# Optimization experiments

Measured on AMD Instinct MI355X. Metric: run time of the kernel, lower is better.

## Reference

```python
import jax, jax.numpy as jnp
import numpy as np

LEAKY_SLOPE = 0.01

def bilinear_interpolate(grid, coords):
    # grid: [H, W, C]; coords: [N, 2] in [0,1] (x, y order as in torch code)
    H = grid.shape[0] - 1
    W = grid.shape[1] - 1
    fx = coords[:, 0] * W
    fy = coords[:, 1] * H
    x0 = fx.astype(jnp.int32)
    y0 = fy.astype(jnp.int32)
    xf = jnp.mod(fx, 1.0)
    yf = jnp.mod(fy, 1.0)
    x1 = jnp.minimum(x0 + 1, W)
    y1 = jnp.minimum(y0 + 1, H)
    tl = grid[y0, x0]  # [N, C]
    tr = grid[y0, x1]
    bl = grid[y1, x0]
    br = grid[y1, x1]
    xf = xf[:, None]
    yf = yf[:, None]
    top = (1.0 - xf) * tl + xf * tr
    bot = (1.0 - xf) * bl + xf * br
    return (1.0 - yf) * top + yf * bot


def setup_inputs() -> dict:
    key = jax.random.key(0)
    ks = jax.random.split(key, 10)
    N = 2097152
    pos = jax.random.uniform(ks[0], (N, 2), dtype=jnp.float32)
    dir = jax.random.uniform(ks[1], (N, 2), dtype=jnp.float32)
    pos_grid = jax.random.normal(ks[2], (256, 256, 3), dtype=jnp.float32) * 10.0
    dir_grid = jax.random.normal(ks[3], (256, 256, 3), dtype=jnp.float32) * 10.0
    # Linear layers: PyTorch default init U(-1/sqrt(fan_in), 1/sqrt(fan_in))
    def linear(kw, kb, fan_in, fan_out):
        bound = 1.0 / np.sqrt(fan_in)
        W = jax.random.uniform(kw, (fan_out, fan_in), minval=-bound, maxval=bound, dtype=jnp.float32)
        b = jax.random.uniform(kb, (fan_out,), minval=-bound, maxval=bound, dtype=jnp.float32)
        return W, b
    W1, b1 = linear(ks[4], ks[5], 6, 64)
    W2, b2 = linear(ks[6], ks[7], 64, 64)
    W3, b3 = linear(ks[8], ks[9], 64, 1)
    return {"pos": pos, "dir": dir, "pos_grid": pos_grid, "dir_grid": dir_grid,
            "W1": W1, "b1": b1, "W2": W2, "b2": b2, "W3": W3, "b3": b3}


def reference(pos, dir, pos_grid, dir_grid, W1, b1, W2, b2, W3, b3):
    pos_feat = jax.lax.stop_gradient(bilinear_interpolate(pos_grid, pos))  # .detach() in torch
    dir_feat = jax.lax.stop_gradient(bilinear_interpolate(dir_grid, dir))
    x = jnp.concatenate([pos_feat, dir_feat], axis=1)  # [N, 6]
    x = jax.nn.leaky_relu(x @ W1.T + b1, LEAKY_SLOPE)
    x = jax.nn.leaky_relu(x @ W2.T + b2, LEAKY_SLOPE)
    return jax.nn.sigmoid(x @ W3.T + b3)  # [N, 1]
```

## Files before the change

### kernel.cpp

```cpp
#include <hip/hip_runtime.h>
#include <hip/hip_bf16.h>
#include <math.h>


#define NTHREADS 256
#define NB 4

typedef __attribute__((ext_vector_type(4))) short s16x4;
typedef __attribute__((ext_vector_type(8))) short s16x8;
typedef __attribute__((ext_vector_type(8))) __bf16 bf16x8;
typedef __attribute__((ext_vector_type(4))) float f32x4;
typedef __attribute__((ext_vector_type(4))) int i32x4;
typedef __attribute__((ext_vector_type(2))) int i32x2;

static __device__ __forceinline__ short f2bf(float f) {
    return __builtin_bit_cast(short, __float2bfloat16(f));
}
static __device__ __forceinline__ int pk2(float lo, float hi) {
    unsigned short l = (unsigned short)f2bf(lo);
    unsigned short h = (unsigned short)f2bf(hi);
    return (int)(((unsigned int)h << 16) | (unsigned int)l);
}
static __device__ __forceinline__ int cvt_pk_bf16(float a, float b) {
    int r;
    asm("v_cvt_pk_bf16_f32 %0, %1, %2" : "=v"(r) : "v"(a), "v"(b));
    return r;
}
static __device__ __forceinline__ float bflo(int u) {
    return __builtin_bit_cast(float, u << 16);
}
static __device__ __forceinline__ float bfhi(int u) {
    return __builtin_bit_cast(float, (int)(u & 0xffff0000));
}
static __device__ __forceinline__ int opaq(int x) {
    asm volatile("" : "+v"(x));
    return x;
}

__global__ __launch_bounds__(256) void make_patches(
    const float* __restrict__ gP, const float* __restrict__ gD,
    int* __restrict__ outP, int* __restrict__ outD) {
    int gid = blockIdx.x * 256 + threadIdx.x;
    const float* g = (gid < 65536) ? gP : gD;
    int* po = (gid < 65536) ? outP : outD;
    int id = gid & 65535;
    int y0 = id >> 8, x0 = id & 255;
    int x1 = min(x0 + 1, 255), y1 = min(y0 + 1, 255);
    const float* tl = g + (y0 * 256 + x0) * 3;
    const float* tr = g + (y0 * 256 + x1) * 3;
    const float* bl = g + (y1 * 256 + x0) * 3;
    const float* br = g + (y1 * 256 + x1) * 3;
    i32x4 u0;
    i32x2 u1;
    u0[0] = pk2(tl[0], bl[0]);
    u0[1] = pk2(tl[1], bl[1]);
    u0[2] = pk2(tl[2], bl[2]);
    u0[3] = pk2(tr[0], br[0]);
    u1[0] = pk2(tr[1], br[1]);
    u1[1] = pk2(tr[2], br[2]);
    *(i32x4*)(po + id * 8) = u0;
    *(i32x2*)(po + id * 8 + 4) = u1;
}

static __device__ __forceinline__ void patch_issue(
    const int* __restrict__ tab, float px, float py, int* P, float& xf,
    float& yf) {
    float fx = px * 255.0f;
    float fy = py * 255.0f;
    int x0 = (int)fx;
    int y0 = (int)fy;
    xf = fx - floorf(fx);
    yf = fy - floorf(fy);
    int idx = (y0 << 8) | x0;
    i32x4 a = *(const i32x4*)(tab + idx * 8);
    i32x2 b = *(const i32x2*)(tab + idx * 8 + 4);
    P[0] = a[0]; P[1] = a[1]; P[2] = a[2];
    P[3] = a[3]; P[4] = b[0]; P[5] = b[1];
}

static __device__ __forceinline__ void patch_lerp(const int* P, float xf,
                                                  float yf, float* f) {
#pragma unroll
    for (int ch = 0; ch < 3; ++ch) {
        float tl = bflo(P[ch]), bl = bfhi(P[ch]);
        float tr = bflo(P[ch + 3]), br = bfhi(P[ch + 3]);
        float top = fmaf(xf, tr - tl, tl);
        float bot = fmaf(xf, br - bl, bl);
        f[ch] = fmaf(yf, bot - top, top);
    }
}

__global__ __launch_bounds__(NTHREADS, 4) void mlp_mfma_kernel(
    const float* __restrict__ pos, const float* __restrict__ dir,
    const int* __restrict__ patP, const int* __restrict__ patD,
    const float* __restrict__ W1, const float* __restrict__ b1,
    const float* __restrict__ W2, const float* __restrict__ b2,
    const float* __restrict__ W3, const float* __restrict__ b3,
    float* __restrict__ out) {
    __shared__ int lds_F[4 * 2 * 64 * 4];
    __shared__ __align__(16) float cw[128];

    const int tid = threadIdx.x;
    if (tid < 128) cw[tid] = (tid < 64) ? b2[tid] : W3[tid - 64];
    __syncthreads();

    const int w = tid >> 6;
    const int lane = tid & 63;
    const int c = lane & 15;
    const int q = lane >> 4;
    const int q4 = q * 4;

    int* FB = lds_F + w * (2 * 64 * 4);

    s16x4 A1f[4];
#pragma unroll
    for (int mt = 0; mt < 4; ++mt) {
        int f = mt * 16 + c;
        s16x4 t;
#pragma unroll
        for (int j = 0; j < 4; ++j) {
            int k = q4 + j;
            float v = 0.0f;
            if (k < 6) v = W1[f * 6 + k];
            else if (k == 6) v = b1[f];
            t[j] = f2bf(v);
        }
        A1f[mt] = t;
    }
    s16x8 A2f[2][4];
#pragma unroll
    for (int kt2 = 0; kt2 < 2; ++kt2)
#pragma unroll
        for (int mt = 0; mt < 4; ++mt) {
            int n2 = mt * 16 + c;
            s16x8 t;
#pragma unroll
            for (int j2 = 0; j2 < 8; ++j2) {
                int k = kt2 * 32 + ((j2 >> 2) * 16) + q4 + (j2 & 3);
                t[j2] = f2bf(W2[n2 * 64 + k]);
            }
            A2f[kt2][mt] = t;
        }
    const float b3s = b3[0];
    const int dbias = pk2(1.0f, 0.0f);
    const f32x4 zacc = {0.f, 0.f, 0.f, 0.f};

    const long wave_global = (long)blockIdx.x * 4 + w;
    const long base0 = wave_global * (64L * NB);
    const float2* pos2 = (const float2*)pos;
    const float2* dir2 = (const float2*)dir;

    float2 cp1, cd1;
    {
        float2 c0p = pos2[base0 + lane], c0d = dir2[base0 + lane];
        cp1 = pos2[base0 + 64 + lane];
        cd1 = dir2[base0 + 64 + lane];
        int P0_[12];
        float fr0[4];
        patch_issue(patP, c0p.x, c0p.y, P0_, fr0[0], fr0[1]);
        patch_issue(patD, c0d.x, c0d.y, P0_ + 6, fr0[2], fr0[3]);
        float feat[6];
        patch_lerp(P0_, fr0[0], fr0[1], feat);
        patch_lerp(P0_ + 6, fr0[2], fr0[3], feat + 3);
        i32x4 dv;
        dv[0] = cvt_pk_bf16(feat[0], feat[1]);
        dv[1] = cvt_pk_bf16(feat[2], feat[3]);
        dv[2] = cvt_pk_bf16(feat[4], feat[5]);
        dv[3] = dbias;
        *(i32x4*)(FB + lane * 4) = dv;
    }

#pragma unroll 1
    for (int ib = 0; ib < NB; ++ib) {
        const long base = base0 + ib * 64;
        const int cur = ib & 1;

        int PB[12];
        float frB[4];
        patch_issue(patP, cp1.x, cp1.y, PB, frB[0], frB[1]);
        patch_issue(patD, cd1.x, cd1.y, PB + 6, frB[2], frB[3]);

        {
            int mb = min(ib + 2, NB - 1);
            cp1 = pos2[base0 + mb * 64 + lane];
            cd1 = dir2[base0 + mb * 64 + lane];
        }

        float s[4];
#pragma unroll
        for (int t = 0; t < 4; ++t) {
            i32x2 bi = *(const i32x2*)(FB + cur * 256 + (t * 16 + c) * 4 +
                                       (q & 1) * 2);
            s16x4 bfeat = __builtin_bit_cast(s16x4, bi);

            f32x4 a1[4];
#pragma unroll
            for (int mt = 0; mt < 4; ++mt)
                a1[mt] = __builtin_amdgcn_mfma_f32_16x16x16bf16_1k(
                    A1f[mt], bfeat, zacc, 0, 0, 0);

            i32x4 bbi[2];
#pragma unroll
            for (int kt2 = 0; kt2 < 2; ++kt2)
#pragma unroll
                for (int h = 0; h < 2; ++h) {
                    f32x4 x = a1[kt2 * 2 + h];
                    float l0 = fmaxf(x[0], 0.01f * x[0]);
                    float l1 = fmaxf(x[1], 0.01f * x[1]);
                    float l2 = fmaxf(x[2], 0.01f * x[2]);
                    float l3 = fmaxf(x[3], 0.01f * x[3]);
                    bbi[kt2][h * 2 + 0] = cvt_pk_bf16(l0, l1);
                    bbi[kt2][h * 2 + 1] = cvt_pk_bf16(l2, l3);
                }

            f32x4 a2[4];
            {
                const float* cwb = cw + opaq(q4);
#pragma unroll
                for (int mt = 0; mt < 4; ++mt)
                    a2[mt] = *(const f32x4*)(cwb + mt * 16);
            }
#pragma unroll
            for (int kt2 = 0; kt2 < 2; ++kt2) {
                bf16x8 bb = __builtin_bit_cast(bf16x8, bbi[kt2]);
#pragma unroll
                for (int mt = 0; mt < 4; ++mt)
                    a2[mt] = __builtin_amdgcn_mfma_f32_16x16x32_bf16(
                        __builtin_bit_cast(bf16x8, A2f[kt2][mt]), bb, a2[mt],
                        0, 0, 0);
            }

            float tx = 0.0f, ta = 0.0f;
            const float* cww = cw + opaq(64 + q4);
#pragma unroll
            for (int mt = 0; mt < 4; ++mt) {
                const f32x4 wv = *(const f32x4*)(cww + mt * 16);
#pragma unroll
                for (int r = 0; r < 4; ++r) {
                    float x = a2[mt][r];
                    tx = fmaf(x, wv[r], tx);
                    ta = fmaf(__builtin_fabsf(x), wv[r], ta);
                }
            }
            float tt = fmaf(0.505f, tx, 0.495f * ta);
            tt += __shfl_xor(tt, 16, 64);
            tt += __shfl_xor(tt, 32, 64);
            s[t] = tt;
        }

        float sa = (q & 1) ? s[1] : s[0];
        float sb = (q & 1) ? s[3] : s[2];
        float v = (q & 2) ? sb : sa;
        v += b3s;
        v = 1.0f / (1.0f + __expf(-v));
        out[base + q * 16 + c] = v;

        {
            float feat[6];
            patch_lerp(PB, frB[0], frB[1], feat);
            patch_lerp(PB + 6, frB[2], frB[3], feat + 3);
            i32x4 dv;
            dv[0] = cvt_pk_bf16(feat[0], feat[1]);
            dv[1] = cvt_pk_bf16(feat[2], feat[3]);
            dv[2] = cvt_pk_bf16(feat[4], feat[5]);
            dv[3] = dbias;
            *(i32x4*)(FB + (cur ^ 1) * 256 + lane * 4) = dv;
        }
    }
}

extern "C" void kernel_launch(void* const* d_in, const int* in_sizes, int n_in,
                              void* d_out, int out_size, void* d_ws,
                              size_t ws_size, hipStream_t stream) {
    const float* pos = (const float*)d_in[0];
    const float* dir = (const float*)d_in[1];
    const float* pos_grid = (const float*)d_in[2];
    const float* dir_grid = (const float*)d_in[3];
    const float* W1 = (const float*)d_in[4];
    const float* b1 = (const float*)d_in[5];
    const float* W2 = (const float*)d_in[6];
    const float* b2 = (const float*)d_in[7];
    const float* W3 = (const float*)d_in[8];
    const float* b3 = (const float*)d_in[9];
    float* out = (float*)d_out;

    int* patP = (int*)d_ws;
    int* patD = patP + 65536 * 8;

    make_patches<<<512, 256, 0, stream>>>(pos_grid, dir_grid, patP, patD);

    const int n = in_sizes[0] / 2;
    const int batches = n / 64;
    const int waves = batches / NB;
    const int blocks = waves / 4;

    mlp_mfma_kernel<<<blocks, NTHREADS, 0, stream>>>(
        pos, dir, patP, patD, W1, b1, W2, b2, W3, b3, out);
}
```

Measured before the change: 147.4 us.

## Prepack MLP weights once and process one 64-point batch per wave

Adds a tiny pack_weights kernel that converts W1/b1/W2 into per-lane bf16 fragment layouts, so the main kernel loads its weights with vector loads instead of gathering and converting them every wave. The main kernel drops the 4-batch software-pipelined loop with double-buffered LDS and handles a single 64-point batch per wave, launching 4x more blocks with a higher occupancy hint. This trades the cross-batch prefetch overlap for more waves and less per-wave setup, and it adds an extra kernel launch.

```diff
diff --git a/kernel.cpp b/kernel.cpp
--- a/kernel.cpp
+++ b/kernel.cpp
@@ -4,7 +4,6 @@
 
 
 #define NTHREADS 256
-#define NB 4
 
 typedef __attribute__((ext_vector_type(4))) short s16x4;
 typedef __attribute__((ext_vector_type(8))) short s16x8;
@@ -62,6 +61,45 @@
     *(i32x2*)(po + id * 8 + 4) = u1;
 }
 
+__global__ void pack_weights(const float* __restrict__ W1,
+                             const float* __restrict__ b1,
+                             const float* __restrict__ W2,
+                             int* __restrict__ wt1, int* __restrict__ wt2) {
+    int lane = threadIdx.x;
+    int c = lane & 15, q = lane >> 4, q4 = q * 4;
+#pragma unroll
+    for (int mt = 0; mt < 4; ++mt) {
+        int f = mt * 16 + c;
+        float v[4];
+#pragma unroll
+        for (int j = 0; j < 4; ++j) {
+            int k = q4 + j;
+            float x = 0.0f;
+            if (k < 6) x = W1[f * 6 + k];
+            else if (k == 6) x = b1[f];
+            v[j] = x;
+        }
+        wt1[lane * 8 + mt * 2 + 0] = pk2(v[0], v[1]);
+        wt1[lane * 8 + mt * 2 + 1] = pk2(v[2], v[3]);
+    }
+#pragma unroll
+    for (int kt2 = 0; kt2 < 2; ++kt2)
+#pragma unroll
+        for (int mt = 0; mt < 4; ++mt) {
+            int n2 = mt * 16 + c;
+            float v[8];
+#pragma unroll
+            for (int j2 = 0; j2 < 8; ++j2) {
+                int k = kt2 * 32 + ((j2 >> 2) * 16) + q4 + (j2 & 3);
+                v[j2] = W2[n2 * 64 + k];
+            }
+            int base = lane * 32 + (kt2 * 4 + mt) * 4;
+#pragma unroll
+            for (int h = 0; h < 4; ++h)
+                wt2[base + h] = pk2(v[2 * h], v[2 * h + 1]);
+        }
+}
+
 static __device__ __forceinline__ void patch_issue(
     const int* __restrict__ tab, float px, float py, int* P, float& xf,
     float& yf) {
@@ -90,14 +128,13 @@
     }
 }
 
-__global__ __launch_bounds__(NTHREADS, 4) void mlp_mfma_kernel(
+__global__ __launch_bounds__(NTHREADS, 5) void mlp_mfma_kernel(
     const float* __restrict__ pos, const float* __restrict__ dir,
     const int* __restrict__ patP, const int* __restrict__ patD,
-    const float* __restrict__ W1, const float* __restrict__ b1,
-    const float* __restrict__ W2, const float* __restrict__ b2,
-    const float* __restrict__ W3, const float* __restrict__ b3,
-    float* __restrict__ out) {
-    __shared__ int lds_F[4 * 2 * 64 * 4];
+    const int* __restrict__ wt1, const int* __restrict__ wt2,
+    const float* __restrict__ b2, const float* __restrict__ W3,
+    const float* __restrict__ b3, float* __restrict__ out) {
+    __shared__ int lds_F[4 * 64 * 4];
     __shared__ __align__(16) float cw[128];
 
     const int tid = threadIdx.x;
@@ -110,55 +147,37 @@
     const int q = lane >> 4;
     const int q4 = q * 4;
 
-    int* FB = lds_F + w * (2 * 64 * 4);
+    int* FB = lds_F + w * (64 * 4);
 
     s16x4 A1f[4];
 #pragma unroll
-    for (int mt = 0; mt < 4; ++mt) {
-        int f = mt * 16 + c;
-        s16x4 t;
-#pragma unroll
-        for (int j = 0; j < 4; ++j) {
-            int k = q4 + j;
-            float v = 0.0f;
-            if (k < 6) v = W1[f * 6 + k];
-            else if (k == 6) v = b1[f];
-            t[j] = f2bf(v);
-        }
-        A1f[mt] = t;
-    }
+    for (int mt = 0; mt < 4; ++mt)
+        A1f[mt] = __builtin_bit_cast(
+            s16x4, *(const i32x2*)(wt1 + lane * 8 + mt * 2));
     s16x8 A2f[2][4];
 #pragma unroll
     for (int kt2 = 0; kt2 < 2; ++kt2)
 #pragma unroll
-        for (int mt = 0; mt < 4; ++mt) {
-            int n2 = mt * 16 + c;
-            s16x8 t;
-#pragma unroll
-            for (int j2 = 0; j2 < 8; ++j2) {
-                int k = kt2 * 32 + ((j2 >> 2) * 16) + q4 + (j2 & 3);
-                t[j2] = f2bf(W2[n2 * 64 + k]);
-            }
-            A2f[kt2][mt] = t;
-        }
+        for (int mt = 0; mt < 4; ++mt)
+            A2f[kt2][mt] = __builtin_bit_cast(
+                s16x8,
+                *(const i32x4*)(wt2 + lane * 32 + (kt2 * 4 + mt) * 4));
+
     const float b3s = b3[0];
     const int dbias = pk2(1.0f, 0.0f);
     const f32x4 zacc = {0.f, 0.f, 0.f, 0.f};
 
-    const long wave_global = (long)blockIdx.x * 4 + w;
-    const long base0 = wave_global * (64L * NB);
+    const long base = ((long)blockIdx.x * 4 + w) * 64;
     const float2* pos2 = (const float2*)pos;
     const float2* dir2 = (const float2*)dir;
 
-    float2 cp1, cd1;
     {
-        float2 c0p = pos2[base0 + lane], c0d = dir2[base0 + lane];
-        cp1 = pos2[base0 + 64 + lane];
-        cd1 = dir2[base0 + 64 + lane];
+        float2 cp = pos2[base + lane];
+        float2 cd = dir2[base + lane];
         int P0_[12];
         float fr0[4];
-        patch_issue(patP, c0p.x, c0p.y, P0_, fr0[0], fr0[1]);
-        patch_issue(patD, c0d.x, c0d.y, P0_ + 6, fr0[2], fr0[3]);
+        patch_issue(patP, cp.x, cp.y, P0_, fr0[0], fr0[1]);
+        patch_issue(patD, cd.x, cd.y, P0_ + 6, fr0[2], fr0[3]);
         float feat[6];
         patch_lerp(P0_, fr0[0], fr0[1], feat);
         patch_lerp(P0_ + 6, fr0[2], fr0[3], feat + 3);
@@ -170,103 +189,73 @@
         *(i32x4*)(FB + lane * 4) = dv;
     }
 
-#pragma unroll 1
-    for (int ib = 0; ib < NB; ++ib) {
-        const long base = base0 + ib * 64;
-        const int cur = ib & 1;
-
-        int PB[12];
-        float frB[4];
-        patch_issue(patP, cp1.x, cp1.y, PB, frB[0], frB[1]);
-        patch_issue(patD, cd1.x, cd1.y, PB + 6, frB[2], frB[3]);
-
+    float s[4];
+#pragma unroll
+    for (int t = 0; t < 4; ++t) {
+        i32x2 bi = *(const i32x2*)(FB + (t * 16 + c) * 4 + (q & 1) * 2);
+        s16x4 bfeat = __builtin_bit_cast(s16x4, bi);
+
+        f32x4 a1[4];
+#pragma unroll
+        for (int mt = 0; mt < 4; ++mt)
+            a1[mt] = __builtin_amdgcn_mfma_f32_16x16x16bf16_1k(
+                A1f[mt], bfeat, zacc, 0, 0, 0);
+
+        i32x4 bbi[2];
+#pragma unroll
+        for (int kt2 = 0; kt2 < 2; ++kt2)
+#pragma unroll
+            for (int h = 0; h < 2; ++h) {
+                f32x4 x = a1[kt2 * 2 + h];
+                float l0 = fmaxf(x[0], 0.01f * x[0]);
+                float l1 = fmaxf(x[1], 0.01f * x[1]);
+                float l2 = fmaxf(x[2], 0.01f * x[2]);
+                float l3 = fmaxf(x[3], 0.01f * x[3]);
+                bbi[kt2][h * 2 + 0] = cvt_pk_bf16(l0, l1);
+                bbi[kt2][h * 2 + 1] = cvt_pk_bf16(l2, l3);
+            }
+
+        f32x4 a2[4];
         {
-            int mb = min(ib + 2, NB - 1);
-            cp1 = pos2[base0 + mb * 64 + lane];
-            cd1 = dir2[base0 + mb * 64 + lane];
-        }
-
-        float s[4];
-#pragma unroll
-        for (int t = 0; t < 4; ++t) {
-            i32x2 bi = *(const i32x2*)(FB + cur * 256 + (t * 16 + c) * 4 +
-                                       (q & 1) * 2);
-            s16x4 bfeat = __builtin_bit_cast(s16x4, bi);
-
-            f32x4 a1[4];
+            const float* cwb = cw + opaq(q4);
 #pragma unroll
             for (int mt = 0; mt < 4; ++mt)
-                a1[mt] = __builtin_amdgcn_mfma_f32_16x16x16bf16_1k(
-                    A1f[mt], bfeat, zacc, 0, 0, 0);
-
-            i32x4 bbi[2];
-#pragma unroll
-            for (int kt2 = 0; kt2 < 2; ++kt2)
-#pragma unroll
-                for (int h = 0; h < 2; ++h) {
-                    f32x4 x = a1[kt2 * 2 + h];
-                    float l0 = fmaxf(x[0], 0.01f * x[0]);
-                    float l1 = fmaxf(x[1], 0.01f * x[1]);
-                    float l2 = fmaxf(x[2], 0.01f * x[2]);
-                    float l3 = fmaxf(x[3], 0.01f * x[3]);
-                    bbi[kt2][h * 2 + 0] = cvt_pk_bf16(l0, l1);
-                    bbi[kt2][h * 2 + 1] = cvt_pk_bf16(l2, l3);
-                }
-
-            f32x4 a2[4];
-            {
-                const float* cwb = cw + opaq(q4);
-#pragma unroll
-                for (int mt = 0; mt < 4; ++mt)
-                    a2[mt] = *(const f32x4*)(cwb + mt * 16);
+                a2[mt] = *(const f32x4*)(cwb + mt * 16);
+        }
+#pragma unroll
+        for (int kt2 = 0; kt2 < 2; ++kt2) {
+            bf16x8 bb = __builtin_bit_cast(bf16x8, bbi[kt2]);
+#pragma unroll
+            for (int mt = 0; mt < 4; ++mt)
+                a2[mt] = __builtin_amdgcn_mfma_f32_16x16x32_bf16(
+                    __builtin_bit_cast(bf16x8, A2f[kt2][mt]), bb, a2[mt],
+                    0, 0, 0);
+        }
+
+        float tx = 0.0f, ta = 0.0f;
+        const float* cww = cw + opaq(64 + q4);
+#pragma unroll
+        for (int mt = 0; mt < 4; ++mt) {
+            const f32x4 wv = *(const f32x4*)(cww + mt * 16);
+#pragma unroll
+            for (int r = 0; r < 4; ++r) {
+                float x = a2[mt][r];
+                tx = fmaf(x, wv[r], tx);
+                ta = fmaf(__builtin_fabsf(x), wv[r], ta);
             }
-#pragma unroll
-            for (int kt2 = 0; kt2 < 2; ++kt2) {
-                bf16x8 bb = __builtin_bit_cast(bf16x8, bbi[kt2]);
-#pragma unroll
-                for (int mt = 0; mt < 4; ++mt)
-                    a2[mt] = __builtin_amdgcn_mfma_f32_16x16x32_bf16(
-                        __builtin_bit_cast(bf16x8, A2f[kt2][mt]), bb, a2[mt],
-                        0, 0, 0);
-            }
-
-            float tx = 0.0f, ta = 0.0f;
-            const float* cww = cw + opaq(64 + q4);
-#pragma unroll
-            for (int mt = 0; mt < 4; ++mt) {
-                const f32x4 wv = *(const f32x4*)(cww + mt * 16);
-#pragma unroll
-                for (int r = 0; r < 4; ++r) {
-                    float x = a2[mt][r];
-                    tx = fmaf(x, wv[r], tx);
-                    ta = fmaf(__builtin_fabsf(x), wv[r], ta);
-                }
-            }
-            float tt = fmaf(0.505f, tx, 0.495f * ta);
-            tt += __shfl_xor(tt, 16, 64);
-            tt += __shfl_xor(tt, 32, 64);
-            s[t] = tt;
-        }
-
-        float sa = (q & 1) ? s[1] : s[0];
-        float sb = (q & 1) ? s[3] : s[2];
-        float v = (q & 2) ? sb : sa;
-        v += b3s;
-        v = 1.0f / (1.0f + __expf(-v));
-        out[base + q * 16 + c] = v;
-
-        {
-            float feat[6];
-            patch_lerp(PB, frB[0], frB[1], feat);
-            patch_lerp(PB + 6, frB[2], frB[3], feat + 3);
-            i32x4 dv;
-            dv[0] = cvt_pk_bf16(feat[0], feat[1]);
-            dv[1] = cvt_pk_bf16(feat[2], feat[3]);
-            dv[2] = cvt_pk_bf16(feat[4], feat[5]);
-            dv[3] = dbias;
-            *(i32x4*)(FB + (cur ^ 1) * 256 + lane * 4) = dv;
-        }
-    }
+        }
+        float tt = fmaf(0.505f, tx, 0.495f * ta);
+        tt += __shfl_xor(tt, 16, 64);
+        tt += __shfl_xor(tt, 32, 64);
+        s[t] = tt;
+    }
+
+    float sa = (q & 1) ? s[1] : s[0];
+    float sb = (q & 1) ? s[3] : s[2];
+    float v = (q & 2) ? sb : sa;
+    v += b3s;
+    v = 1.0f / (1.0f + __expf(-v));
+    out[base + q * 16 + c] = v;
 }
 
 extern "C" void kernel_launch(void* const* d_in, const int* in_sizes, int n_in,
@@ -286,14 +275,16 @@
 
     int* patP = (int*)d_ws;
     int* patD = patP + 65536 * 8;
+    int* wt1 = patD + 65536 * 8;
+    int* wt2 = wt1 + 512;
 
     make_patches<<<512, 256, 0, stream>>>(pos_grid, dir_grid, patP, patD);
+    pack_weights<<<1, 64, 0, stream>>>(W1, b1, W2, wt1, wt2);
 
     const int n = in_sizes[0] / 2;
     const int batches = n / 64;
-    const int waves = batches / NB;
-    const int blocks = waves / 4;
+    const int blocks = batches / 4;
 
     mlp_mfma_kernel<<<blocks, NTHREADS, 0, stream>>>(
-        pos, dir, patP, patD, W1, b1, W2, b2, W3, b3, out);
-}
+        pos, dir, patP, patD, wt1, wt2, b2, W3, b3, out);
+}
```

New measurement: 154.5 us. 4.8% more time.
